# Kernel tuning notes

Measured on AMD Instinct MI355X. Metric: run time of the kernel, lower is better.

The kernel has to match this reference:

```python
import jax, jax.numpy as jnp
import numpy as np

N_U = 8192
N_C = 8192
D_IN = 32
D_HID = 32  # hidden_dim == output_dim (required by the concat->Linear shape)


def _glorot(key, fan_in, fan_out):
    r = np.sqrt(6.0 / (fan_in + fan_out)).astype(np.float32)
    return jax.random.uniform(key, (fan_in, fan_out), jnp.float32, -r, r)


def setup_inputs() -> dict:
    key = jax.random.key(0)
    ks = jax.random.split(key, 12)
    X_U = jax.random.normal(ks[0], (N_U, D_IN), jnp.float32)
    X_C = jax.random.normal(ks[1], (N_C, D_IN), jnp.float32)
    adj_uu = jax.random.uniform(ks[2], (N_U, N_U), jnp.float32)
    adj_uc = jax.random.uniform(ks[3], (N_U, N_C), jnp.float32)
    adj_cc = jax.random.uniform(ks[4], (N_C, N_C), jnp.float32)
    weight_s = _glorot(ks[5], D_IN, D_HID)          # GCN_S.weight (shared for uu and cc)
    proj_u = _glorot(ks[6], D_IN, D_HID)            # GCN_C.projection_u
    proj_c = _glorot(ks[7], D_IN, D_HID)            # GCN_C.projection_c (unused in fwd math)
    weight_c = _glorot(ks[8], D_HID, D_HID)         # GCN_C.weight
    W_lin = jax.random.normal(ks[9], (D_IN + D_HID, D_HID), jnp.float32) * 0.05  # Linear, no bias
    a_vec = jax.random.normal(ks[10], (D_HID, 1), jnp.float32) * 0.05            # attention vector
    return {"X_U": X_U, "X_C": X_C, "adj_uu": adj_uu, "adj_uc": adj_uc, "adj_cc": adj_cc,
            "weight_s": weight_s, "proj_u": proj_u, "proj_c": proj_c,
            "weight_c": weight_c, "W_lin": W_lin, "a_vec": a_vec}


def gcn_s(adj, x, w):
    # D^-1/2 A D^-1/2 (X W), with D = 1 + rowsum(A); expressed as broadcast scaling
    dinv = jax.lax.rsqrt(1.0 + jnp.sum(adj, axis=1))  # [N]
    support = x @ w                                    # [N, d]
    return dinv[:, None] * (adj @ (dinv[:, None] * support))


def gcn_c(adj, x_u, p_u, w):
    # Du^-1/2 A Dc^-1/2 ((X_U P_u) W); projected_c is computed but unused upstream
    du = jax.lax.rsqrt(jnp.sum(adj, axis=1))  # [N_u]
    dc = jax.lax.rsqrt(jnp.sum(adj, axis=0))  # [N_c]
    support = (x_u @ p_u) @ w                  # [N_u, d]
    return du[:, None] * (adj @ (dc[:, None] * support))  # wait: see note below


def gcn_c_correct(adj, x_u, p_u, w):
    # norm_adj = diag(du) @ adj @ diag(dc)  -> [N_u, N_c]; output = norm_adj @ support ([N_u,d])
    # Actually original multiplies [N_u,N_c] norm_adj by support built from X_U [N_u,d]:
    # this only typechecks when N_u == N_c (as in the repo's usage). We keep that math.
    du = jax.lax.rsqrt(jnp.sum(adj, axis=1))
    dc = jax.lax.rsqrt(jnp.sum(adj, axis=0))
    support = (x_u @ p_u) @ w
    return du[:, None] * (adj @ (dc[:, None] * support))


def reference(X_U, X_C, adj_uu, adj_uc, adj_cc, weight_s, proj_u, proj_c, weight_c, W_lin, a_vec):
    node_embed_u = gcn_s(adj_uu, X_U, weight_s)            # [N_u, d]
    node_embed_c1 = gcn_s(adj_cc, X_C, weight_s)           # [N_c, d]
    node_embed_c2 = gcn_c_correct(adj_uc, X_U, proj_u, weight_c)  # [N_c, d]

    a_tau_1 = jax.nn.relu(jnp.concatenate([node_embed_c1, X_C], axis=-1) @ W_lin) @ a_vec  # [N_c,1]
    a_tau_2 = jax.nn.relu(jnp.concatenate([node_embed_c2, X_C], axis=-1) @ W_lin) @ a_vec  # [N_c,1]
    e_tau = jax.nn.softmax(jnp.concatenate([a_tau_1, a_tau_2], axis=1), axis=1)            # [N_c,2]

    Y_c = e_tau[:, 0:1] * node_embed_c1
    Y_u = e_tau[:, 1:2] * node_embed_c2
    node_embed_c = Y_c + Y_u
    return (node_embed_u, node_embed_c, Y_c, Y_u)
```

## Files before the change

kernel.cpp:

```cpp
#include <hip/hip_runtime.h>
#include <hip/hip_bf16.h>

#define N_NODES 8192

typedef __attribute__((ext_vector_type(8))) short short8;
typedef __attribute__((ext_vector_type(8))) unsigned short ushort8;
typedef __attribute__((ext_vector_type(4))) unsigned short ushort4v;
typedef __attribute__((ext_vector_type(4))) float floatx4;

__device__ inline unsigned short f2bf(float f) {
  unsigned int u = __float_as_uint(f);
  u = (u + 0x7FFFu + ((u >> 16) & 1u)) >> 16;
  return (unsigned short)u;
}

__device__ inline float waveSum(float s) {
#pragma unroll
  for (int off = 32; off >= 1; off >>= 1) s += __shfl_xor(s, off, 64);
  return s;
}

__device__ inline void acc4(float4& a, const float4 b) {
  a.x += b.x; a.y += b.y; a.z += b.z; a.w += b.w;
}
__device__ inline float hsum4(const float4 v) { return v.x + v.y + v.z + v.w; }

__global__ __launch_bounds__(256) void k_rowsum(const float* __restrict__ a_uu,
                                                const float* __restrict__ a_cc,
                                                float* __restrict__ dinv_uu,
                                                float* __restrict__ dinv_cc) {
  const float* A = (blockIdx.y == 0) ? a_uu : a_cc;
  float* dv = (blockIdx.y == 0) ? dinv_uu : dinv_cc;
  int w = threadIdx.x >> 6, l = threadIdx.x & 63;
  long row = (long)blockIdx.x * 4 + w;
  const float* rp = A + row * N_NODES + 4 * l;
  float s = 0.f;
#pragma unroll 2
  for (int i = 0; i < 32; i += 4) {
    float4 v0 = *(const float4*)(rp + 256 * (i + 0));
    float4 v1 = *(const float4*)(rp + 256 * (i + 1));
    float4 v2 = *(const float4*)(rp + 256 * (i + 2));
    float4 v3 = *(const float4*)(rp + 256 * (i + 3));
    s += hsum4(v0) + hsum4(v1) + hsum4(v2) + hsum4(v3);
  }
  s = waveSum(s);
  if (l == 0) dv[row] = rsqrtf(1.0f + s);
}

__global__ __launch_bounds__(256) void k_uc_partials(const float* __restrict__ adj,
                                                     float* __restrict__ rs_part,
                                                     float* __restrict__ cs_part) {
  __shared__ float cacc[4][1024];
  int t = threadIdx.x, w = t >> 6, l = t & 63;
  int rc = blockIdx.x, cc = blockIdx.y;
  int c0 = cc * 1024;
  int rbase = rc * 128 + w * 32;
  float4 ca0 = {0, 0, 0, 0}, ca1 = {0, 0, 0, 0}, ca2 = {0, 0, 0, 0}, ca3 = {0, 0, 0, 0};
  for (int kr = 0; kr < 32; kr += 2) {
    const float* p0 = adj + (long)(rbase + kr) * N_NODES + c0 + 4 * l;
    const float* p1 = p0 + N_NODES;
    float4 u0 = *(const float4*)(p0 + 0);
    float4 u1 = *(const float4*)(p0 + 256);
    float4 u2 = *(const float4*)(p0 + 512);
    float4 u3 = *(const float4*)(p0 + 768);
    float4 v0 = *(const float4*)(p1 + 0);
    float4 v1 = *(const float4*)(p1 + 256);
    float4 v2 = *(const float4*)(p1 + 512);
    float4 v3 = *(const float4*)(p1 + 768);
    acc4(ca0, u0); acc4(ca1, u1); acc4(ca2, u2); acc4(ca3, u3);
    acc4(ca0, v0); acc4(ca1, v1); acc4(ca2, v2); acc4(ca3, v3);
    float s0 = hsum4(u0) + hsum4(u1) + hsum4(u2) + hsum4(u3);
    float s1 = hsum4(v0) + hsum4(v1) + hsum4(v2) + hsum4(v3);
    s0 = waveSum(s0);
    s1 = waveSum(s1);
    if (l == 0) {
      rs_part[(long)cc * N_NODES + rbase + kr] = s0;
      rs_part[(long)cc * N_NODES + rbase + kr + 1] = s1;
    }
  }
  *(float4*)&cacc[w][0 + 4 * l] = ca0;
  *(float4*)&cacc[w][256 + 4 * l] = ca1;
  *(float4*)&cacc[w][512 + 4 * l] = ca2;
  *(float4*)&cacc[w][768 + 4 * l] = ca3;
  __syncthreads();
#pragma unroll
  for (int i = 0; i < 4; ++i) {
    int c = t + 256 * i;
    cs_part[(long)rc * N_NODES + c0 + c] = cacc[0][c] + cacc[1][c] + cacc[2][c] + cacc[3][c];
  }
}

__global__ __launch_bounds__(256) void k_finalize(const float* __restrict__ rs_part,
                                                  const float* __restrict__ cs_part,
                                                  float* __restrict__ du,
                                                  float* __restrict__ dc) {
  int i = blockIdx.x * 256 + threadIdx.x;
  float s = 0.f;
#pragma unroll
  for (int cc = 0; cc < 8; ++cc) s += rs_part[(long)cc * N_NODES + i];
  du[i] = rsqrtf(s);
  float c = 0.f;
#pragma unroll
  for (int rc = 0; rc < 64; ++rc) c += cs_part[(long)rc * N_NODES + i];
  dc[i] = rsqrtf(c);
}

__global__ void k_projw(const float* __restrict__ proj_u,
                        const float* __restrict__ weight_c, float* __restrict__ P) {
  int t = threadIdx.x;
  int i = t >> 5, j = t & 31;
  float s = 0.f;
#pragma unroll
  for (int k = 0; k < 32; ++k) s += proj_u[i * 32 + k] * weight_c[k * 32 + j];
  P[t] = s;
}

__global__ __launch_bounds__(256) void k_support(
    const float* __restrict__ X_U, const float* __restrict__ X_C,
    const float* __restrict__ weight_s, const float* __restrict__ P,
    const float* __restrict__ dinv_uu, const float* __restrict__ dinv_cc,
    const float* __restrict__ dc,
    unsigned short* __restrict__ bt_uu, unsigned short* __restrict__ bt_cc,
    unsigned short* __restrict__ bt_uc) {
  int m = blockIdx.y;
  const float* X = (m == 1) ? X_C : X_U;
  const float* W = (m == 2) ? P : weight_s;
  const float* dv = (m == 0) ? dinv_uu : (m == 1) ? dinv_cc : dc;
  unsigned short* bt = (m == 0) ? bt_uu : (m == 1) ? bt_cc : bt_uc;
  __shared__ float Wl[32][32];
  __shared__ float Xl[8][32];
  int t = threadIdx.x;
#pragma unroll
  for (int i = 0; i < 4; ++i) {
    int idx = t + 256 * i;
    Wl[idx >> 5][idx & 31] = W[idx];
  }
  int r = t >> 5, n = t & 31;
  int j0 = blockIdx.x * 8;
  Xl[r][n] = X[(long)(j0 + r) * 32 + n];
  __syncthreads();
  float s = 0.f;
#pragma unroll
  for (int k = 0; k < 32; ++k) s += Xl[r][k] * Wl[k][n];
  s *= dv[j0 + r];
  bt[(long)n * N_NODES + j0 + r] = f2bf(s);
}

__global__ __launch_bounds__(256) void k_gemm(
    const float* __restrict__ adj_uu, const float* __restrict__ adj_cc,
    const float* __restrict__ adj_uc,
    const unsigned short* __restrict__ bt_uu, const unsigned short* __restrict__ bt_cc,
    const unsigned short* __restrict__ bt_uc,
    const float* __restrict__ dinv_uu, const float* __restrict__ dinv_cc,
    const float* __restrict__ du,
    float* __restrict__ out_u, float* __restrict__ c1, float* __restrict__ c2) {
  int m = blockIdx.y;
  const float* adj = (m == 0) ? adj_uu : (m == 1) ? adj_cc : adj_uc;
  const unsigned short* bt = (m == 0) ? bt_uu : (m == 1) ? bt_cc : bt_uc;
  const float* dsc = (m == 0) ? dinv_uu : (m == 1) ? dinv_cc : du;
  float* outp = (m == 0) ? out_u : (m == 1) ? c1 : c2;

  __shared__ unsigned short As[32][136];
  __shared__ unsigned short Bs[32][136];

  int t = threadIdx.x;
  int w = t >> 6, l = t & 63;
  int mh = w & 1, nh = w >> 1;
  long r0 = (long)blockIdx.x * 32;

  int ar = t >> 3, ac = (t & 7) * 4;
  int bn = t >> 3, bk = (t & 7) * 8;

  const float* ap = adj + (r0 + ar) * N_NODES + ac;
  const unsigned short* bp = bt + (long)bn * N_NODES + bk;

  float4 a0 = *(const float4*)(ap + 0);
  float4 a1 = *(const float4*)(ap + 32);
  float4 a2 = *(const float4*)(ap + 64);
  float4 a3 = *(const float4*)(ap + 96);
  ushort8 b0 = *(const ushort8*)(bp + 0);
  ushort8 b1 = *(const ushort8*)(bp + 64);

  floatx4 acc = {0.f, 0.f, 0.f, 0.f};

  for (int step = 0; step < 64; ++step) {
    ushort4v q;
    q.x = f2bf(a0.x); q.y = f2bf(a0.y); q.z = f2bf(a0.z); q.w = f2bf(a0.w);
    *(ushort4v*)&As[ar][ac + 0] = q;
    q.x = f2bf(a1.x); q.y = f2bf(a1.y); q.z = f2bf(a1.z); q.w = f2bf(a1.w);
    *(ushort4v*)&As[ar][ac + 32] = q;
    q.x = f2bf(a2.x); q.y = f2bf(a2.y); q.z = f2bf(a2.z); q.w = f2bf(a2.w);
    *(ushort4v*)&As[ar][ac + 64] = q;
    q.x = f2bf(a3.x); q.y = f2bf(a3.y); q.z = f2bf(a3.z); q.w = f2bf(a3.w);
    *(ushort4v*)&As[ar][ac + 96] = q;
    *(ushort8*)&Bs[bn][bk + 0] = b0;
    *(ushort8*)&Bs[bn][bk + 64] = b1;
    __syncthreads();

    if (step < 63) {
      ap += 128; bp += 128;
      a0 = *(const float4*)(ap + 0);
      a1 = *(const float4*)(ap + 32);
      a2 = *(const float4*)(ap + 64);
      a3 = *(const float4*)(ap + 96);
      b0 = *(const ushort8*)(bp + 0);
      b1 = *(const ushort8*)(bp + 64);
    }

#pragma unroll
    for (int kk = 0; kk < 4; ++kk) {
      short8 af = *(const short8*)&As[16 * mh + (l & 15)][kk * 32 + (l >> 4) * 8];
      short8 bf = *(const short8*)&Bs[16 * nh + (l & 15)][kk * 32 + (l >> 4) * 8];
      acc = __builtin_amdgcn_mfma_f32_16x16x32_bf16(af, bf, acc, 0, 0, 0);
    }
    __syncthreads();
  }

  int mrow = (int)r0 + 16 * mh + ((l >> 4) << 2);
  int ncol = 16 * nh + (l & 15);
#pragma unroll
  for (int r = 0; r < 4; ++r) {
    float sc = dsc[mrow + r];
    outp[(long)(mrow + r) * 32 + ncol] = sc * acc[r];
  }
}

__global__ __launch_bounds__(256) void k_epilogue(
    const float* __restrict__ c1, const float* __restrict__ c2,
    const float* __restrict__ X_C, const float* __restrict__ W_lin,
    const float* __restrict__ a_vec, float* __restrict__ out) {
  __shared__ float Wl[64][32];
  __shared__ float al[32];
  int t = threadIdx.x;
#pragma unroll
  for (int i = 0; i < 8; ++i) {
    int idx = t + 256 * i;
    Wl[idx >> 5][idx & 31] = W_lin[idx];
  }
  if (t < 32) al[t] = a_vec[t];
  int g = t >> 5, n = t & 31;
  long row = (long)blockIdx.x * 8 + g;
  __syncthreads();
  float h1 = c1[row * 32 + n];
  float h2 = c2[row * 32 + n];
  float xv = X_C[row * 32 + n];
  float s1 = 0.f, s2 = 0.f, sx = 0.f;
#pragma unroll
  for (int k = 0; k < 32; ++k) {
    float h1k = __shfl(h1, k, 32);
    float h2k = __shfl(h2, k, 32);
    float xk = __shfl(xv, k, 32);
    float w0 = Wl[k][n], w1 = Wl[32 + k][n];
    s1 += h1k * w0;
    s2 += h2k * w0;
    sx += xk * w1;
  }
  float t1 = fmaxf(s1 + sx, 0.f) * al[n];
  float t2 = fmaxf(s2 + sx, 0.f) * al[n];
#pragma unroll
  for (int off = 16; off >= 1; off >>= 1) {
    t1 += __shfl_xor(t1, off, 32);
    t2 += __shfl_xor(t2, off, 32);
  }
  float mx = fmaxf(t1, t2);
  float e1 = expf(t1 - mx), e2 = expf(t2 - mx);
  float inv = 1.0f / (e1 + e2);
  float w1w = e1 * inv, w2w = e2 * inv;
  float yc = w1w * h1, yu = w2w * h2;
  long o = row * 32 + n;
  out[262144 + o] = yc + yu;
  out[524288 + o] = yc;
  out[786432 + o] = yu;
}

extern "C" void kernel_launch(void* const* d_in, const int* in_sizes, int n_in,
                              void* d_out, int out_size, void* d_ws, size_t ws_size,
                              hipStream_t stream) {
  (void)in_sizes; (void)n_in; (void)out_size; (void)ws_size;
  const float* X_U = (const float*)d_in[0];
  const float* X_C = (const float*)d_in[1];
  const float* adj_uu = (const float*)d_in[2];
  const float* adj_uc = (const float*)d_in[3];
  const float* adj_cc = (const float*)d_in[4];
  const float* weight_s = (const float*)d_in[5];
  const float* proj_u = (const float*)d_in[6];
  const float* weight_c = (const float*)d_in[8];
  const float* W_lin = (const float*)d_in[9];
  const float* a_vec = (const float*)d_in[10];
  float* out = (float*)d_out;

  char* ws = (char*)d_ws;
  auto alloc = [&](size_t bytes) {
    char* p = ws;
    ws += (bytes + 255) & ~(size_t)255;
    return p;
  };
  float* dinv_uu = (float*)alloc(8192 * 4);
  float* dinv_cc = (float*)alloc(8192 * 4);
  float* du = (float*)alloc(8192 * 4);
  float* dc = (float*)alloc(8192 * 4);
  float* rs_part = (float*)alloc((size_t)8 * 8192 * 4);
  float* cs_part = (float*)alloc((size_t)64 * 8192 * 4);
  float* P = (float*)alloc(1024 * 4);
  float* c1 = (float*)alloc((size_t)262144 * 4);
  float* c2 = (float*)alloc((size_t)262144 * 4);
  unsigned short* bt_uu = (unsigned short*)alloc((size_t)262144 * 2);
  unsigned short* bt_cc = (unsigned short*)alloc((size_t)262144 * 2);
  unsigned short* bt_uc = (unsigned short*)alloc((size_t)262144 * 2);

  hipLaunchKernelGGL(k_rowsum, dim3(2048, 2), dim3(256), 0, stream,
                     adj_uu, adj_cc, dinv_uu, dinv_cc);
  hipLaunchKernelGGL(k_uc_partials, dim3(64, 8), dim3(256), 0, stream,
                     adj_uc, rs_part, cs_part);
  hipLaunchKernelGGL(k_finalize, dim3(32), dim3(256), 0, stream,
                     rs_part, cs_part, du, dc);
  hipLaunchKernelGGL(k_projw, dim3(1), dim3(1024), 0, stream, proj_u, weight_c, P);
  hipLaunchKernelGGL(k_support, dim3(1024, 3), dim3(256), 0, stream,
                     X_U, X_C, weight_s, P, dinv_uu, dinv_cc, dc, bt_uu, bt_cc, bt_uc);
  hipLaunchKernelGGL(k_gemm, dim3(256, 3), dim3(256), 0, stream,
                     adj_uu, adj_cc, adj_uc, bt_uu, bt_cc, bt_uc,
                     dinv_uu, dinv_cc, du, out, c1, c2);
  hipLaunchKernelGGL(k_epilogue, dim3(1024), dim3(256), 0, stream,
                     c1, c2, X_C, W_lin, a_vec, out);
}
```

Measured before the change: 862.7 us.

## Merge degree kernels with atomics and load GEMM operands directly into registers

Replaces the separate row-sum, uc-partials and finalize reductions with a single k_degree kernel that handles all three adjacency matrices; column sums for adj_uc are accumulated with atomicAdd into a zeroed buffer. The GEMM drops its LDS staging and barriers: each lane loads its MFMA fragments straight from global memory, double-buffered in registers, and converts to bf16 in place. This removes the partial-sum traffic and synchronization, but the GEMM now issues narrower, less coalesced global loads. The degree kernel also issues many contended atomics.

```diff
diff --git a/kernel.cpp b/kernel.cpp
--- a/kernel.cpp
+++ b/kernel.cpp
@@ -25,84 +25,69 @@
 }
 __device__ inline float hsum4(const float4 v) { return v.x + v.y + v.z + v.w; }
 
-__global__ __launch_bounds__(256) void k_rowsum(const float* __restrict__ a_uu,
-                                                const float* __restrict__ a_cc,
-                                                float* __restrict__ dinv_uu,
-                                                float* __restrict__ dinv_cc) {
-  const float* A = (blockIdx.y == 0) ? a_uu : a_cc;
-  float* dv = (blockIdx.y == 0) ? dinv_uu : dinv_cc;
-  int w = threadIdx.x >> 6, l = threadIdx.x & 63;
-  long row = (long)blockIdx.x * 4 + w;
-  const float* rp = A + row * N_NODES + 4 * l;
-  float s = 0.f;
+__device__ inline short8 cvt8(const float4 lo, const float4 hi) {
+  short8 r;
+  r[0] = (short)f2bf(lo.x); r[1] = (short)f2bf(lo.y);
+  r[2] = (short)f2bf(lo.z); r[3] = (short)f2bf(lo.w);
+  r[4] = (short)f2bf(hi.x); r[5] = (short)f2bf(hi.y);
+  r[6] = (short)f2bf(hi.z); r[7] = (short)f2bf(hi.w);
+  return r;
+}
+
+__global__ __launch_bounds__(256) void k_degree(
+    const float* __restrict__ a_uu, const float* __restrict__ a_cc,
+    const float* __restrict__ a_uc,
+    float* __restrict__ dinv_uu, float* __restrict__ dinv_cc,
+    float* __restrict__ du, float* __restrict__ cs) {
+  const int y = blockIdx.y;
+  const float* A = (y == 0) ? a_uu : (y == 1) ? a_cc : a_uc;
+  const bool uc = (y == 2);
+  int t = threadIdx.x, w = t >> 6, l = t & 63;
+  long r0 = (long)blockIdx.x * 32;
+  __shared__ float rp_lds[32][4];
+
+  float4 colacc[8];
+#pragma unroll
+  for (int m = 0; m < 8; ++m) colacc[m] = (float4){0.f, 0.f, 0.f, 0.f};
+
 #pragma unroll 2
-  for (int i = 0; i < 32; i += 4) {
-    float4 v0 = *(const float4*)(rp + 256 * (i + 0));
-    float4 v1 = *(const float4*)(rp + 256 * (i + 1));
-    float4 v2 = *(const float4*)(rp + 256 * (i + 2));
-    float4 v3 = *(const float4*)(rp + 256 * (i + 3));
-    s += hsum4(v0) + hsum4(v1) + hsum4(v2) + hsum4(v3);
-  }
-  s = waveSum(s);
-  if (l == 0) dv[row] = rsqrtf(1.0f + s);
-}
-
-__global__ __launch_bounds__(256) void k_uc_partials(const float* __restrict__ adj,
-                                                     float* __restrict__ rs_part,
-                                                     float* __restrict__ cs_part) {
-  __shared__ float cacc[4][1024];
-  int t = threadIdx.x, w = t >> 6, l = t & 63;
-  int rc = blockIdx.x, cc = blockIdx.y;
-  int c0 = cc * 1024;
-  int rbase = rc * 128 + w * 32;
-  float4 ca0 = {0, 0, 0, 0}, ca1 = {0, 0, 0, 0}, ca2 = {0, 0, 0, 0}, ca3 = {0, 0, 0, 0};
-  for (int kr = 0; kr < 32; kr += 2) {
-    const float* p0 = adj + (long)(rbase + kr) * N_NODES + c0 + 4 * l;
-    const float* p1 = p0 + N_NODES;
-    float4 u0 = *(const float4*)(p0 + 0);
-    float4 u1 = *(const float4*)(p0 + 256);
-    float4 u2 = *(const float4*)(p0 + 512);
-    float4 u3 = *(const float4*)(p0 + 768);
-    float4 v0 = *(const float4*)(p1 + 0);
-    float4 v1 = *(const float4*)(p1 + 256);
-    float4 v2 = *(const float4*)(p1 + 512);
-    float4 v3 = *(const float4*)(p1 + 768);
-    acc4(ca0, u0); acc4(ca1, u1); acc4(ca2, u2); acc4(ca3, u3);
-    acc4(ca0, v0); acc4(ca1, v1); acc4(ca2, v2); acc4(ca3, v3);
-    float s0 = hsum4(u0) + hsum4(u1) + hsum4(u2) + hsum4(u3);
-    float s1 = hsum4(v0) + hsum4(v1) + hsum4(v2) + hsum4(v3);
-    s0 = waveSum(s0);
-    s1 = waveSum(s1);
-    if (l == 0) {
-      rs_part[(long)cc * N_NODES + rbase + kr] = s0;
-      rs_part[(long)cc * N_NODES + rbase + kr + 1] = s1;
+  for (int r = 0; r < 32; ++r) {
+    const float* rowp = A + (r0 + r) * N_NODES + 4 * t;
+    float4 v[8];
+#pragma unroll
+    for (int m = 0; m < 8; ++m) v[m] = *(const float4*)(rowp + 1024 * m);
+    float rp = 0.f;
+#pragma unroll
+    for (int m = 0; m < 8; ++m) {
+      rp += hsum4(v[m]);
+      if (uc) acc4(colacc[m], v[m]);
     }
-  }
-  *(float4*)&cacc[w][0 + 4 * l] = ca0;
-  *(float4*)&cacc[w][256 + 4 * l] = ca1;
-  *(float4*)&cacc[w][512 + 4 * l] = ca2;
-  *(float4*)&cacc[w][768 + 4 * l] = ca3;
+    rp = waveSum(rp);
+    if (l == 0) rp_lds[r][w] = rp;
+  }
   __syncthreads();
-#pragma unroll
-  for (int i = 0; i < 4; ++i) {
-    int c = t + 256 * i;
-    cs_part[(long)rc * N_NODES + c0 + c] = cacc[0][c] + cacc[1][c] + cacc[2][c] + cacc[3][c];
-  }
-}
-
-__global__ __launch_bounds__(256) void k_finalize(const float* __restrict__ rs_part,
-                                                  const float* __restrict__ cs_part,
-                                                  float* __restrict__ du,
+  if (t < 32) {
+    float s = rp_lds[t][0] + rp_lds[t][1] + rp_lds[t][2] + rp_lds[t][3];
+    if (y == 0) dinv_uu[r0 + t] = rsqrtf(1.0f + s);
+    else if (y == 1) dinv_cc[r0 + t] = rsqrtf(1.0f + s);
+    else du[r0 + t] = rsqrtf(s);
+  }
+  if (uc) {
+#pragma unroll
+    for (int m = 0; m < 8; ++m) {
+      float* cp = cs + 4 * t + 1024 * m;
+      atomicAdd(cp + 0, colacc[m].x);
+      atomicAdd(cp + 1, colacc[m].y);
+      atomicAdd(cp + 2, colacc[m].z);
+      atomicAdd(cp + 3, colacc[m].w);
+    }
+  }
+}
+
+__global__ __launch_bounds__(256) void k_finalize(const float* __restrict__ cs,
                                                   float* __restrict__ dc) {
   int i = blockIdx.x * 256 + threadIdx.x;
-  float s = 0.f;
-#pragma unroll
-  for (int cc = 0; cc < 8; ++cc) s += rs_part[(long)cc * N_NODES + i];
-  du[i] = rsqrtf(s);
-  float c = 0.f;
-#pragma unroll
-  for (int rc = 0; rc < 64; ++rc) c += cs_part[(long)rc * N_NODES + i];
-  dc[i] = rsqrtf(c);
+  dc[i] = rsqrtf(cs[i]);
 }
 
 __global__ void k_projw(const float* __restrict__ proj_u,
@@ -160,61 +145,43 @@
   const float* dsc = (m == 0) ? dinv_uu : (m == 1) ? dinv_cc : du;
   float* outp = (m == 0) ? out_u : (m == 1) ? c1 : c2;
 
-  __shared__ unsigned short As[32][136];
-  __shared__ unsigned short Bs[32][136];
-
   int t = threadIdx.x;
   int w = t >> 6, l = t & 63;
   int mh = w & 1, nh = w >> 1;
   long r0 = (long)blockIdx.x * 32;
 
-  int ar = t >> 3, ac = (t & 7) * 4;
-  int bn = t >> 3, bk = (t & 7) * 8;
-
-  const float* ap = adj + (r0 + ar) * N_NODES + ac;
-  const unsigned short* bp = bt + (long)bn * N_NODES + bk;
-
-  float4 a0 = *(const float4*)(ap + 0);
-  float4 a1 = *(const float4*)(ap + 32);
-  float4 a2 = *(const float4*)(ap + 64);
-  float4 a3 = *(const float4*)(ap + 96);
-  ushort8 b0 = *(const ushort8*)(bp + 0);
-  ushort8 b1 = *(const ushort8*)(bp + 64);
+  const float* pa = adj + (r0 + 16 * mh + (l & 15)) * (long)N_NODES + ((l >> 4) * 8);
+  const short* pb = (const short*)bt + (long)(16 * nh + (l & 15)) * N_NODES + ((l >> 4) * 8);
 
   floatx4 acc = {0.f, 0.f, 0.f, 0.f};
 
-  for (int step = 0; step < 64; ++step) {
-    ushort4v q;
-    q.x = f2bf(a0.x); q.y = f2bf(a0.y); q.z = f2bf(a0.z); q.w = f2bf(a0.w);
-    *(ushort4v*)&As[ar][ac + 0] = q;
-    q.x = f2bf(a1.x); q.y = f2bf(a1.y); q.z = f2bf(a1.z); q.w = f2bf(a1.w);
-    *(ushort4v*)&As[ar][ac + 32] = q;
-    q.x = f2bf(a2.x); q.y = f2bf(a2.y); q.z = f2bf(a2.z); q.w = f2bf(a2.w);
-    *(ushort4v*)&As[ar][ac + 64] = q;
-    q.x = f2bf(a3.x); q.y = f2bf(a3.y); q.z = f2bf(a3.z); q.w = f2bf(a3.w);
-    *(ushort4v*)&As[ar][ac + 96] = q;
-    *(ushort8*)&Bs[bn][bk + 0] = b0;
-    *(ushort8*)&Bs[bn][bk + 64] = b1;
-    __syncthreads();
-
-    if (step < 63) {
-      ap += 128; bp += 128;
-      a0 = *(const float4*)(ap + 0);
-      a1 = *(const float4*)(ap + 32);
-      a2 = *(const float4*)(ap + 64);
-      a3 = *(const float4*)(ap + 96);
-      b0 = *(const ushort8*)(bp + 0);
-      b1 = *(const ushort8*)(bp + 64);
+  float4 a0[8]; short8 b0[4];
+  float4 a1[8]; short8 b1[4];
+
+#define LOAD_TILE(A_, B_, OFF)                                        \
+  _Pragma("unroll") for (int kk = 0; kk < 4; ++kk) {                  \
+    A_[2 * kk]     = *(const float4*)(pa + (OFF) + kk * 32);          \
+    A_[2 * kk + 1] = *(const float4*)(pa + (OFF) + kk * 32 + 4);      \
+    B_[kk]         = *(const short8*)(pb + (OFF) + kk * 32);          \
+  }
+
+#define COMPUTE_TILE(A_, B_)                                          \
+  _Pragma("unroll") for (int kk = 0; kk < 4; ++kk) {                  \
+    short8 af = cvt8(A_[2 * kk], A_[2 * kk + 1]);                     \
+    acc = __builtin_amdgcn_mfma_f32_16x16x32_bf16(af, B_[kk], acc, 0, 0, 0); \
+  }
+
+  LOAD_TILE(a0, b0, 0)
+  for (int step = 0; step < 64; step += 2) {
+    LOAD_TILE(a1, b1, (step + 1) * 128)
+    COMPUTE_TILE(a0, b0)
+    if (step + 2 < 64) {
+      LOAD_TILE(a0, b0, (step + 2) * 128)
     }
-
-#pragma unroll
-    for (int kk = 0; kk < 4; ++kk) {
-      short8 af = *(const short8*)&As[16 * mh + (l & 15)][kk * 32 + (l >> 4) * 8];
-      short8 bf = *(const short8*)&Bs[16 * nh + (l & 15)][kk * 32 + (l >> 4) * 8];
-      acc = __builtin_amdgcn_mfma_f32_16x16x32_bf16(af, bf, acc, 0, 0, 0);
-    }
-    __syncthreads();
-  }
+    COMPUTE_TILE(a1, b1)
+  }
+#undef LOAD_TILE
+#undef COMPUTE_TILE
 
   int mrow = (int)r0 + 16 * mh + ((l >> 4) << 2);
   int ncol = 16 * nh + (l & 15);
@@ -299,8 +266,7 @@
   float* dinv_cc = (float*)alloc(8192 * 4);
   float* du = (float*)alloc(8192 * 4);
   float* dc = (float*)alloc(8192 * 4);
-  float* rs_part = (float*)alloc((size_t)8 * 8192 * 4);
-  float* cs_part = (float*)alloc((size_t)64 * 8192 * 4);
+  float* cs = (float*)alloc(8192 * 4);
   float* P = (float*)alloc(1024 * 4);
   float* c1 = (float*)alloc((size_t)262144 * 4);
   float* c2 = (float*)alloc((size_t)262144 * 4);
@@ -308,12 +274,10 @@
   unsigned short* bt_cc = (unsigned short*)alloc((size_t)262144 * 2);
   unsigned short* bt_uc = (unsigned short*)alloc((size_t)262144 * 2);
 
-  hipLaunchKernelGGL(k_rowsum, dim3(2048, 2), dim3(256), 0, stream,
-                     adj_uu, adj_cc, dinv_uu, dinv_cc);
-  hipLaunchKernelGGL(k_uc_partials, dim3(64, 8), dim3(256), 0, stream,
-                     adj_uc, rs_part, cs_part);
-  hipLaunchKernelGGL(k_finalize, dim3(32), dim3(256), 0, stream,
-                     rs_part, cs_part, du, dc);
+  hipMemsetAsync(cs, 0, 8192 * 4, stream);
+  hipLaunchKernelGGL(k_degree, dim3(256, 3), dim3(256), 0, stream,
+                     adj_uu, adj_cc, adj_uc, dinv_uu, dinv_cc, du, cs);
+  hipLaunchKernelGGL(k_finalize, dim3(32), dim3(256), 0, stream, cs, dc);
   hipLaunchKernelGGL(k_projw, dim3(1), dim3(1024), 0, stream, proj_u, weight_c, P);
   hipLaunchKernelGGL(k_support, dim3(1024, 3), dim3(256), 0, stream,
                      X_U, X_C, weight_s, P, dinv_uu, dinv_cc, dc, bt_uu, bt_cc, bt_uc);
```

After: 960.1 us. 11.3% more time.
